# Kernel tuning notes

Hardware: AMD Instinct MI355X
Metric: run time of the kernel (lower is better)

The kernel has to match this reference:

```python
import jax, jax.numpy as jnp
import numpy as np

HIDDEN = 512
QK_DIM = HIDDEN // 8  # 64
B, H, W = 32, 32, 32


def conv1x1(x, w, b):
    # 1x1 conv == channel matmul: w [out_c, in_c], x [b, in_c, h, w]
    return jnp.einsum('oc,bchw->bohw', w, x) + b[None, :, None, None]


def setup_inputs() -> dict:
    key = jax.random.key(0)
    ks = jax.random.split(key, 10)
    s = 0.02
    return {
        'x': jax.random.normal(ks[0], (B, HIDDEN, H, W), jnp.float32),
        'pos_embedding': jax.random.normal(ks[1], (1, HIDDEN, 32, 32), jnp.float32),
        'query_w': jax.random.normal(ks[2], (QK_DIM, HIDDEN), jnp.float32) * s,
        'query_b': jax.random.normal(ks[3], (QK_DIM,), jnp.float32) * s,
        'key_w': jax.random.normal(ks[4], (QK_DIM, HIDDEN), jnp.float32) * s,
        'key_b': jax.random.normal(ks[5], (QK_DIM,), jnp.float32) * s,
        'value_w': jax.random.normal(ks[6], (HIDDEN, HIDDEN), jnp.float32) * s,
        'value_b': jax.random.normal(ks[7], (HIDDEN,), jnp.float32) * s,
        'out_w': jax.random.normal(ks[8], (HIDDEN, HIDDEN), jnp.float32) * s,
        'out_b': jax.random.normal(ks[9], (HIDDEN,), jnp.float32) * s,
    }


def reference(x, pos_embedding, query_w, query_b, key_w, key_b,
              value_w, value_b, out_w, out_b):
    b, c, h, w = x.shape
    n = h * w
    x = x + pos_embedding[:, :, :h, :w]
    q = conv1x1(x, query_w, query_b).reshape(b, -1, n)   # [b, d, n]
    k = conv1x1(x, key_w, key_b).reshape(b, -1, n)       # [b, d, n]
    v = conv1x1(x, value_w, value_b).reshape(b, -1, n)   # [b, c, n]
    # scores[b,i,j] = sum_d q[b,d,i] * k[b,d,j]  (no 1/sqrt(d) scaling, faithful)
    scores = jnp.einsum('bdi,bdj->bij', q, k)
    attn = jax.nn.softmax(scores, axis=-1)               # [b, n, n]
    # out[b,c,i] = sum_j v[b,c,j] * attn[b,i,j]
    out = jnp.einsum('bcj,bij->bci', v, attn).reshape(b, c, h, w)
    return conv1x1(out, out_w, out_b)
```

## Files before the change

kernel.cpp:

```cpp
#include <hip/hip_runtime.h>

#define BB 32
#define CC 512
#define DD 64
#define NN 1024
#define GRP 16
#define NGRP (BB / GRP)

typedef float4 f4;
typedef __attribute__((ext_vector_type(8))) short bf16x8;
typedef __attribute__((ext_vector_type(4))) float f32x4;
typedef __attribute__((ext_vector_type(4))) unsigned short us4;
typedef __attribute__((ext_vector_type(8))) unsigned short us8;

__device__ inline unsigned short bf16rn(float f) {
  union { float f; unsigned u; } v; v.f = f;
  unsigned r = v.u + 0x7fff + ((v.u >> 16) & 1);
  return (unsigned short)(r >> 16);
}

__device__ inline void gl_lds16(const void* g, void* l) {
  __builtin_amdgcn_global_load_lds(
      (const __attribute__((address_space(1))) unsigned int*)g,
      (__attribute__((address_space(3))) unsigned int*)l, 16, 0, 0);
}

__device__ inline void wait_vm0_barrier() {
  asm volatile("s_waitcnt vmcnt(0)" ::: "memory");
  __builtin_amdgcn_s_barrier();
}

__device__ inline int xcd_swz(int bid, int nwg) {
  return (bid & 7) * (nwg >> 3) + (bid >> 3);
}

template <int KDIM>
__device__ inline void gemm_core(const unsigned short* __restrict__ A,
                                 const unsigned short* __restrict__ Bt,
                                 int m0, int n0, int tid,
                                 unsigned short* sA, unsigned short* sB,
                                 f32x4 acc[4][4]) {
  const int wave = tid >> 6, lane = tid & 63;
  const int wm = (wave & 1) * 64, wn = (wave >> 1) * 64;
  const int fm = lane & 15;
  const int kq = lane >> 4;
  const int srow = lane >> 3;
  const int sg   = (lane & 7) ^ srow;

  const unsigned short* ga = A  + (size_t)(m0 + srow) * KDIM + sg * 8;
  const unsigned short* gb = Bt + (size_t)(n0 + srow) * KDIM + sg * 8;

  auto stage = [&](int buf, int k0) {
#pragma unroll
    for (int t = 0; t < 4; ++t) {
      const int R = wave * 32 + t * 8;
      gl_lds16(ga + (size_t)R * KDIM + k0, sA + buf * 8192 + R * 64);
      gl_lds16(gb + (size_t)R * KDIM + k0, sB + buf * 8192 + R * 64);
    }
  };

  stage(0, 0);
  wait_vm0_barrier();

  int cur = 0;
  for (int k0 = 0; k0 < KDIM; k0 += 64) {
    if (k0 + 64 < KDIM) stage(cur ^ 1, k0 + 64);
    const unsigned short* pA = sA + cur * 8192;
    const unsigned short* pB = sB + cur * 8192;
#pragma unroll
    for (int ks = 0; ks < 2; ++ks) {
      bf16x8 af[4], bfr[4];
#pragma unroll
      for (int i = 0; i < 4; ++i) {
        const int ra = wm + i * 16 + fm;
        const int rb = wn + i * 16 + fm;
        af[i]  = *(const bf16x8*)(pA + ra * 64 + ((ks * 4 + kq) ^ (ra & 7)) * 8);
        bfr[i] = *(const bf16x8*)(pB + rb * 64 + ((ks * 4 + kq) ^ (rb & 7)) * 8);
      }
#pragma unroll
      for (int i = 0; i < 4; ++i)
#pragma unroll
        for (int j = 0; j < 4; ++j)
          acc[i][j] = __builtin_amdgcn_mfma_f32_16x16x32_bf16(af[i], bfr[j], acc[i][j], 0, 0, 0);
    }
    wait_vm0_barrier();
    cur ^= 1;
  }
}

__global__ __launch_bounds__(256) void prep_w(
    const float* __restrict__ qw, const float* __restrict__ kw, const float* __restrict__ vw,
    const float* __restrict__ qb, const float* __restrict__ kb, const float* __restrict__ vb,
    const float* __restrict__ ow,
    unsigned short* __restrict__ wcat, unsigned short* __restrict__ owb,
    float* __restrict__ bcat) {
  int idx = blockIdx.x * 256 + threadIdx.x;
  if (idx < 640 * 512) {
    int row = idx >> 9;
    float v = (row < 64) ? qw[idx] : (row < 128) ? kw[idx - 64 * 512] : vw[idx - 128 * 512];
    wcat[idx] = bf16rn(v);
    if (idx < 640) bcat[idx] = (idx < 64) ? qb[idx] : (idx < 128) ? kb[idx - 64] : vb[idx - 128];
  } else {
    int j = idx - 640 * 512;
    owb[j] = bf16rn(ow[j]);
  }
}

__global__ __launch_bounds__(256) void prep_x(const float* __restrict__ x,
                                              const float* __restrict__ pos,
                                              unsigned short* __restrict__ A) {
  __shared__ float t[64][65];
  const int b = blockIdx.z, i0 = blockIdx.x * 64, c0 = blockIdx.y * 64;
  const int tid = threadIdx.x;
  const int ci = tid >> 4, il = (tid & 15) * 4;
  const float* xb = x + (size_t)b * CC * NN;
#pragma unroll
  for (int r = 0; r < 4; ++r) {
    int cl = r * 16 + ci;
    f4 xv = *(const f4*)(xb  + (size_t)(c0 + cl) * NN + i0 + il);
    f4 pv = *(const f4*)(pos + (size_t)(c0 + cl) * NN + i0 + il);
    t[cl][il + 0] = xv.x + pv.x;
    t[cl][il + 1] = xv.y + pv.y;
    t[cl][il + 2] = xv.z + pv.z;
    t[cl][il + 3] = xv.w + pv.w;
  }
  __syncthreads();
  const int iw = tid >> 2, cw = (tid & 3) * 16;
  unsigned short* dst = A + ((size_t)b * NN + i0 + iw) * CC + c0 + cw;
  us8 p0, p1;
#pragma unroll
  for (int j = 0; j < 8; ++j) p0[j] = bf16rn(t[cw + j][iw]);
#pragma unroll
  for (int j = 0; j < 8; ++j) p1[j] = bf16rn(t[cw + 8 + j][iw]);
  *(us8*)dst = p0;
  *(us8*)(dst + 8) = p1;
}

__global__ __launch_bounds__(256) void proj_gemm(
    const unsigned short* __restrict__ A, const unsigned short* __restrict__ wcat,
    const float* __restrict__ bcat,
    unsigned short* __restrict__ qo, unsigned short* __restrict__ ko,
    unsigned short* __restrict__ vto) {
  __shared__ unsigned short sA[16384], sB[16384];
  const int wid = xcd_swz(blockIdx.x, 1280);
  const int m0 = (wid & 7) * 128, n0 = ((wid >> 3) % 5) * 128, b = wid / 40;
  const int tid = threadIdx.x, wave = tid >> 6, lane = tid & 63;
  f32x4 acc[4][4];
#pragma unroll
  for (int i = 0; i < 4; ++i)
#pragma unroll
    for (int j = 0; j < 4; ++j) acc[i][j] = (f32x4)(0.0f);

  gemm_core<512>(A + (size_t)b * NN * CC, wcat, m0, n0, tid, sA, sB, acc);

  const int wm = (wave & 1) * 64, wn = (wave >> 1) * 64;
#pragma unroll
  for (int i = 0; i < 4; ++i)
#pragma unroll
    for (int j = 0; j < 4; ++j) {
      int col  = n0 + wn + j * 16 + (lane & 15);
      int rowb = m0 + wm + i * 16 + (lane >> 4) * 4;
      float bias = bcat[col];
      if (col < 64) {
#pragma unroll
        for (int r = 0; r < 4; ++r)
          qo[((size_t)b * NN + rowb + r) * DD + col] = bf16rn(acc[i][j][r] + bias);
      } else if (col < 128) {
#pragma unroll
        for (int r = 0; r < 4; ++r)
          ko[((size_t)b * NN + rowb + r) * DD + col - 64] = bf16rn(acc[i][j][r] + bias);
      } else {
        int c = col - 128;
        us4 pk;
#pragma unroll
        for (int r = 0; r < 4; ++r) pk[r] = bf16rn(acc[i][j][r] + bias);
        *(us4*)(vto + ((size_t)b * CC + c) * NN + rowb) = pk;
      }
    }
}

__global__ __launch_bounds__(256) void stats_kernel(
    const unsigned short* __restrict__ q, const unsigned short* __restrict__ k,
    float2* __restrict__ stats_part) {
  __shared__ unsigned short sQ[8192];
  __shared__ unsigned short sK[16384];
  __shared__ float2 wred[4][128];

  const int wid = xcd_swz(blockIdx.x, 512);
  const int i0 = (wid & 7) * 128, jc = (wid >> 3) & 1, b = wid >> 4;
  const int jbase = jc * 512;
  const int tid = threadIdx.x, wave = tid >> 6, lane = tid & 63;
  const int wm = (wave & 1) * 64, wn = (wave >> 1) * 64;
  const int fm = lane & 15, kq = lane >> 4;
  const int srow = lane >> 3, sg = (lane & 7) ^ srow;

  const unsigned short* qb = q + (size_t)b * NN * DD;
  const unsigned short* kb = k + (size_t)b * NN * DD;

  auto stageK = [&](int buf, int j0) {
#pragma unroll
    for (int t = 0; t < 4; ++t) {
      const int R = wave * 32 + t * 8;
      gl_lds16(kb + (size_t)(j0 + R + srow) * DD + sg * 8, sK + buf * 8192 + R * 64);
    }
  };

#pragma unroll
  for (int t = 0; t < 4; ++t) {
    const int R = wave * 32 + t * 8;
    gl_lds16(qb + (size_t)(i0 + R + srow) * DD + sg * 8, sQ + R * 64);
  }
  stageK(0, jbase);
  wait_vm0_barrier();

  bf16x8 aq[4][2];
#pragma unroll
  for (int i = 0; i < 4; ++i)
#pragma unroll
    for (int kd = 0; kd < 2; ++kd) {
      const int ra = wm + i * 16 + fm;
      aq[i][kd] = *(const bf16x8*)(sQ + ra * 64 + ((kd * 4 + kq) ^ (ra & 7)) * 8);
    }

  float m_l[4][4], l_l[4][4];
#pragma unroll
  for (int i = 0; i < 4; ++i)
#pragma unroll
    for (int r = 0; r < 4; ++r) { m_l[i][r] = -1e30f; l_l[i][r] = 0.f; }

  int cur = 0;
#pragma unroll
  for (int jt = 0; jt < 4; ++jt) {
    if (jt < 3) stageK(cur ^ 1, jbase + (jt + 1) * 128);
    const unsigned short* pK = sK + cur * 8192;
    f32x4 S[4][4];
#pragma unroll
    for (int i = 0; i < 4; ++i)
#pragma unroll
      for (int j = 0; j < 4; ++j) S[i][j] = (f32x4)(0.0f);
#pragma unroll
    for (int kd = 0; kd < 2; ++kd) {
      bf16x8 bk[4];
#pragma unroll
      for (int j = 0; j < 4; ++j) {
        const int rb = wn + j * 16 + fm;
        bk[j] = *(const bf16x8*)(pK + rb * 64 + ((kd * 4 + kq) ^ (rb & 7)) * 8);
      }
#pragma unroll
      for (int i = 0; i < 4; ++i)
#pragma unroll
        for (int j = 0; j < 4; ++j)
          S[i][j] = __builtin_amdgcn_mfma_f32_16x16x32_bf16(aq[i][kd], bk[j], S[i][j], 0, 0, 0);
    }
#pragma unroll
    for (int i = 0; i < 4; ++i)
#pragma unroll
      for (int r = 0; r < 4; ++r) {
        float v0 = S[i][0][r], v1 = S[i][1][r], v2 = S[i][2][r], v3 = S[i][3][r];
        float mt = fmaxf(fmaxf(v0, v1), fmaxf(v2, v3));
        float lt = __expf(v0 - mt) + __expf(v1 - mt) + __expf(v2 - mt) + __expf(v3 - mt);
        float mo = m_l[i][r];
        float mn = fmaxf(mo, mt);
        l_l[i][r] = l_l[i][r] * __expf(mo - mn) + lt * __expf(mt - mn);
        m_l[i][r] = mn;
      }
    wait_vm0_barrier();
    cur ^= 1;
  }

#pragma unroll
  for (int i = 0; i < 4; ++i)
#pragma unroll
    for (int r = 0; r < 4; ++r) {
      float m = m_l[i][r], l = l_l[i][r];
#pragma unroll
      for (int off = 1; off < 16; off <<= 1) {
        float mo = __shfl_xor(m, off, 64);
        float lo = __shfl_xor(l, off, 64);
        float mn = fmaxf(m, mo);
        l = l * __expf(m - mn) + lo * __expf(mo - mn);
        m = mn;
      }
      m_l[i][r] = m; l_l[i][r] = l;
    }
  if ((lane & 15) == 0) {
#pragma unroll
    for (int i = 0; i < 4; ++i)
#pragma unroll
      for (int r = 0; r < 4; ++r) {
        float2 p; p.x = m_l[i][r]; p.y = l_l[i][r];
        wred[wave][wm + i * 16 + kq * 4 + r] = p;
      }
  }
  __syncthreads();
  if (tid < 128) {
    const int a = tid >> 6;
    float2 p0 = wred[a][tid], p1 = wred[a + 2][tid];
    float mn = fmaxf(p0.x, p1.x);
    float l = p0.y * __expf(p0.x - mn) + p1.y * __expf(p1.x - mn);
    float2 o; o.x = mn; o.y = l;
    stats_part[((size_t)b * NN + i0 + tid) * 2 + jc] = o;
  }
}

__global__ __launch_bounds__(256) void pnorm_kernel(
    const unsigned short* __restrict__ q, const unsigned short* __restrict__ k,
    const float2* __restrict__ stats_part, unsigned short* __restrict__ P) {
  __shared__ unsigned short sQ[8192];
  __shared__ unsigned short sK[8192];

  const int wid = xcd_swz(blockIdx.x, 8 * 8 * GRP);
  const int j0 = (wid & 7) * 128, i0 = ((wid >> 3) & 7) * 128, b = wid >> 6;
  const int tid = threadIdx.x, wave = tid >> 6, lane = tid & 63;
  const int wm = (wave & 1) * 64, wn = (wave >> 1) * 64;
  const int fm = lane & 15, kq = lane >> 4;
  const int srow = lane >> 3, sg = (lane & 7) ^ srow;

  const unsigned short* qb = q + (size_t)b * NN * DD;
  const unsigned short* kb = k + (size_t)b * NN * DD;

#pragma unroll
  for (int t = 0; t < 4; ++t) {
    const int R = wave * 32 + t * 8;
    gl_lds16(qb + (size_t)(i0 + R + srow) * DD + sg * 8, sQ + R * 64);
    gl_lds16(kb + (size_t)(j0 + R + srow) * DD + sg * 8, sK + R * 64);
  }

  float mrow[4][4], irow[4][4];
#pragma unroll
  for (int i = 0; i < 4; ++i)
#pragma unroll
    for (int r = 0; r < 4; ++r) {
      const size_t row = (size_t)b * NN + i0 + wm + i * 16 + kq * 4 + r;
      f4 st = *(const f4*)(stats_part + row * 2);
      float m = fmaxf(st.x, st.z);
      float l = st.y * __expf(st.x - m) + st.w * __expf(st.z - m);
      mrow[i][r] = m; irow[i][r] = 1.0f / l;
    }

  wait_vm0_barrier();

  bf16x8 aq[4][2];
#pragma unroll
  for (int i = 0; i < 4; ++i)
#pragma unroll
    for (int kd = 0; kd < 2; ++kd) {
      const int ra = wm + i * 16 + fm;
      aq[i][kd] = *(const bf16x8*)(sQ + ra * 64 + ((kd * 4 + kq) ^ (ra & 7)) * 8);
    }

  f32x4 S[4][4];
#pragma unroll
  for (int i = 0; i < 4; ++i)
#pragma unroll
    for (int j = 0; j < 4; ++j) S[i][j] = (f32x4)(0.0f);
#pragma unroll
  for (int kd = 0; kd < 2; ++kd) {
    bf16x8 bk[4];
#pragma unroll
    for (int j = 0; j < 4; ++j) {
      const int rb = wn + j * 16 + fm;
      bk[j] = *(const bf16x8*)(sK + rb * 64 + ((kd * 4 + kq) ^ (rb & 7)) * 8);
    }
#pragma unroll
    for (int i = 0; i < 4; ++i)
#pragma unroll
      for (int j = 0; j < 4; ++j)
        S[i][j] = __builtin_amdgcn_mfma_f32_16x16x32_bf16(aq[i][kd], bk[j], S[i][j], 0, 0, 0);
  }
#pragma unroll
  for (int i = 0; i < 4; ++i)
#pragma unroll
    for (int j = 0; j < 4; ++j) {
      const int col = j0 + wn + j * 16 + fm;
#pragma unroll
      for (int r = 0; r < 4; ++r) {
        const int row = i0 + wm + i * 16 + kq * 4 + r;
        P[((size_t)b * NN + row) * NN + col] =
            bf16rn(__expf(S[i][j][r] - mrow[i][r]) * irow[i][r]);
      }
    }
}

__global__ __launch_bounds__(256) void pv_gemm(
    const unsigned short* __restrict__ P, const unsigned short* __restrict__ vT,
    unsigned short* __restrict__ attnout) {
  __shared__ unsigned short sA[16384], sB[16384];
  const int wid = xcd_swz(blockIdx.x, 8 * 4 * GRP);
  const int m0 = (wid & 7) * 128, n0 = ((wid >> 3) & 3) * 128, b = wid >> 5;
  const int tid = threadIdx.x, wave = tid >> 6, lane = tid & 63;
  f32x4 acc[4][4];
#pragma unroll
  for (int i = 0; i < 4; ++i)
#pragma unroll
    for (int j = 0; j < 4; ++j) acc[i][j] = (f32x4)(0.0f);

  gemm_core<1024>(P + (size_t)b * NN * NN, vT + (size_t)b * CC * NN, m0, n0, tid, sA, sB, acc);

  const int wm = (wave & 1) * 64, wn = (wave >> 1) * 64;
#pragma unroll
  for (int i = 0; i < 4; ++i)
#pragma unroll
    for (int j = 0; j < 4; ++j) {
      int col  = n0 + wn + j * 16 + (lane & 15);
      int rowb = m0 + wm + i * 16 + (lane >> 4) * 4;
#pragma unroll
      for (int r = 0; r < 4; ++r)
        attnout[((size_t)b * NN + rowb + r) * CC + col] = bf16rn(acc[i][j][r]);
    }
}

__global__ __launch_bounds__(256) void outproj_gemm(
    const unsigned short* __restrict__ owb, const unsigned short* __restrict__ attnout,
    const float* __restrict__ ob, float* __restrict__ out) {
  __shared__ unsigned short sA[16384], sB[16384];
  const int wid = xcd_swz(blockIdx.x, 1024);
  const int m0 = (wid & 3) * 128, n0 = ((wid >> 2) & 7) * 128, b = wid >> 5;
  const int tid = threadIdx.x, wave = tid >> 6, lane = tid & 63;
  f32x4 acc[4][4];
#pragma unroll
  for (int i = 0; i < 4; ++i)
#pragma unroll
    for (int j = 0; j < 4; ++j) acc[i][j] = (f32x4)(0.0f);

  gemm_core<512>(owb, attnout + (size_t)b * NN * CC, m0, n0, tid, sA, sB, acc);

  const int wm = (wave & 1) * 64, wn = (wave >> 1) * 64;
#pragma unroll
  for (int i = 0; i < 4; ++i)
#pragma unroll
    for (int j = 0; j < 4; ++j) {
      int col  = n0 + wn + j * 16 + (lane & 15);
      int rowb = m0 + wm + i * 16 + (lane >> 4) * 4;
      f4 b4 = *(const f4*)(ob + rowb);
#pragma unroll
      for (int r = 0; r < 4; ++r)
        out[((size_t)b * CC + rowb + r) * NN + col] = acc[i][j][r] + ((const float*)&b4)[r];
    }
}

extern "C" void kernel_launch(void* const* d_in, const int* in_sizes, int n_in,
                              void* d_out, int out_size, void* d_ws, size_t ws_size,
                              hipStream_t stream) {
  const float* x   = (const float*)d_in[0];
  const float* pos = (const float*)d_in[1];
  const float* qw  = (const float*)d_in[2];
  const float* qb  = (const float*)d_in[3];
  const float* kw  = (const float*)d_in[4];
  const float* kb  = (const float*)d_in[5];
  const float* vw  = (const float*)d_in[6];
  const float* vb  = (const float*)d_in[7];
  const float* ow  = (const float*)d_in[8];
  const float* ob  = (const float*)d_in[9];
  float* out = (float*)d_out;

  char* w = (char*)d_ws;
  unsigned short* wcat = (unsigned short*)w; w += (size_t)640 * 512 * 2;
  unsigned short* owb  = (unsigned short*)w; w += (size_t)512 * 512 * 2;
  float*          bcat = (float*)w;          w += 640 * 4;
  unsigned short* A    = (unsigned short*)w; w += (size_t)BB * NN * CC * 2;
  unsigned short* q    = (unsigned short*)w; w += (size_t)BB * NN * DD * 2;
  unsigned short* k    = (unsigned short*)w; w += (size_t)BB * NN * DD * 2;
  unsigned short* vT   = (unsigned short*)w; w += (size_t)BB * CC * NN * 2;
  float2*    stats_prt = (float2*)w;         w += (size_t)BB * NN * 2 * 8;
  unsigned short* PG   = (unsigned short*)w; w += (size_t)GRP * NN * NN * 2;
  unsigned short* attnout = A;

  hipLaunchKernelGGL(prep_w, dim3(2304), dim3(256), 0, stream,
                     qw, kw, vw, qb, kb, vb, ow, wcat, owb, bcat);
  hipLaunchKernelGGL(prep_x, dim3(16, 8, 32), dim3(256), 0, stream, x, pos, A);
  hipLaunchKernelGGL(proj_gemm, dim3(1280), dim3(256), 0, stream,
                     A, wcat, bcat, q, k, vT);
  hipLaunchKernelGGL(stats_kernel, dim3(512), dim3(256), 0, stream, q, k, stats_prt);

  for (int g = 0; g < NGRP; ++g) {
    const unsigned short* qg  = q  + (size_t)g * GRP * NN * DD;
    const unsigned short* kg  = k  + (size_t)g * GRP * NN * DD;
    const unsigned short* vTg = vT + (size_t)g * GRP * CC * NN;
    const float2*         stg = stats_prt + (size_t)g * GRP * NN * 2;
    unsigned short* aog = attnout + (size_t)g * GRP * NN * CC;
    hipLaunchKernelGGL(pnorm_kernel, dim3(8 * 8 * GRP), dim3(256), 0, stream,
                       qg, kg, stg, PG);
    hipLaunchKernelGGL(pv_gemm, dim3(8 * 4 * GRP), dim3(256), 0, stream, PG, vTg, aog);
  }

  hipLaunchKernelGGL(outproj_gemm, dim3(1024), dim3(256), 0, stream,
                     owb, attnout, ob, out);
}
```

Measured before the change: 291.5 us.

## Drop max-subtraction softmax pass; compute exp(QK) once and normalize in PV epilogue

```diff
diff --git a/kernel.cpp b/kernel.cpp
--- a/kernel.cpp
+++ b/kernel.cpp
@@ -179,14 +179,14 @@
     }
 }
 
-__global__ __launch_bounds__(256) void stats_kernel(
+__global__ __launch_bounds__(256) void qkexp_kernel(
     const unsigned short* __restrict__ q, const unsigned short* __restrict__ k,
-    float2* __restrict__ stats_part) {
+    float* __restrict__ lpart, unsigned short* __restrict__ P) {
   __shared__ unsigned short sQ[8192];
   __shared__ unsigned short sK[16384];
-  __shared__ float2 wred[4][128];
-
-  const int wid = xcd_swz(blockIdx.x, 512);
+  __shared__ float wred[4][128];
+
+  const int wid = xcd_swz(blockIdx.x, 8 * 2 * GRP);
   const int i0 = (wid & 7) * 128, jc = (wid >> 3) & 1, b = wid >> 4;
   const int jbase = jc * 512;
   const int tid = threadIdx.x, wave = tid >> 6, lane = tid & 63;
@@ -222,11 +222,7 @@
       aq[i][kd] = *(const bf16x8*)(sQ + ra * 64 + ((kd * 4 + kq) ^ (ra & 7)) * 8);
     }
 
-  float m_l[4][4], l_l[4][4];
-#pragma unroll
-  for (int i = 0; i < 4; ++i)
-#pragma unroll
-    for (int r = 0; r < 4; ++r) { m_l[i][r] = -1e30f; l_l[i][r] = 0.f; }
+  float l_l[4] = {0.f, 0.f, 0.f, 0.f};
 
   int cur = 0;
 #pragma unroll
@@ -235,156 +231,69 @@
     const unsigned short* pK = sK + cur * 8192;
     f32x4 S[4][4];
 #pragma unroll
-    for (int i = 0; i < 4; ++i)
-#pragma unroll
-      for (int j = 0; j < 4; ++j) S[i][j] = (f32x4)(0.0f);
+    for (int jk = 0; jk < 4; ++jk)
+#pragma unroll
+      for (int iq = 0; iq < 4; ++iq) S[jk][iq] = (f32x4)(0.0f);
 #pragma unroll
     for (int kd = 0; kd < 2; ++kd) {
       bf16x8 bk[4];
 #pragma unroll
-      for (int j = 0; j < 4; ++j) {
-        const int rb = wn + j * 16 + fm;
-        bk[j] = *(const bf16x8*)(pK + rb * 64 + ((kd * 4 + kq) ^ (rb & 7)) * 8);
+      for (int jk = 0; jk < 4; ++jk) {
+        const int rb = wn + jk * 16 + fm;
+        bk[jk] = *(const bf16x8*)(pK + rb * 64 + ((kd * 4 + kq) ^ (rb & 7)) * 8);
       }
 #pragma unroll
-      for (int i = 0; i < 4; ++i)
-#pragma unroll
-        for (int j = 0; j < 4; ++j)
-          S[i][j] = __builtin_amdgcn_mfma_f32_16x16x32_bf16(aq[i][kd], bk[j], S[i][j], 0, 0, 0);
-    }
-#pragma unroll
-    for (int i = 0; i < 4; ++i)
-#pragma unroll
-      for (int r = 0; r < 4; ++r) {
-        float v0 = S[i][0][r], v1 = S[i][1][r], v2 = S[i][2][r], v3 = S[i][3][r];
-        float mt = fmaxf(fmaxf(v0, v1), fmaxf(v2, v3));
-        float lt = __expf(v0 - mt) + __expf(v1 - mt) + __expf(v2 - mt) + __expf(v3 - mt);
-        float mo = m_l[i][r];
-        float mn = fmaxf(mo, mt);
-        l_l[i][r] = l_l[i][r] * __expf(mo - mn) + lt * __expf(mt - mn);
-        m_l[i][r] = mn;
+      for (int jk = 0; jk < 4; ++jk)
+#pragma unroll
+        for (int iq = 0; iq < 4; ++iq)
+          S[jk][iq] = __builtin_amdgcn_mfma_f32_16x16x32_bf16(bk[jk], aq[iq][kd], S[jk][iq], 0, 0, 0);
+    }
+    us4 pk[4][4];
+#pragma unroll
+    for (int jk = 0; jk < 4; ++jk)
+#pragma unroll
+      for (int iq = 0; iq < 4; ++iq) {
+#pragma unroll
+        for (int r = 0; r < 4; ++r) {
+          float e = __expf(S[jk][iq][r]);
+          pk[jk][iq][r] = bf16rn(e);
+          l_l[iq] += e;
+        }
       }
     wait_vm0_barrier();
+#pragma unroll
+    for (int jk = 0; jk < 4; ++jk)
+#pragma unroll
+      for (int iq = 0; iq < 4; ++iq) {
+        const int row = i0 + wm + iq * 16 + fm;
+        const int col = jbase + jt * 128 + wn + jk * 16 + kq * 4;
+        *(us4*)(P + ((size_t)b * NN + row) * NN + col) = pk[jk][iq];
+      }
     cur ^= 1;
   }
 
 #pragma unroll
-  for (int i = 0; i < 4; ++i)
-#pragma unroll
-    for (int r = 0; r < 4; ++r) {
-      float m = m_l[i][r], l = l_l[i][r];
-#pragma unroll
-      for (int off = 1; off < 16; off <<= 1) {
-        float mo = __shfl_xor(m, off, 64);
-        float lo = __shfl_xor(l, off, 64);
-        float mn = fmaxf(m, mo);
-        l = l * __expf(m - mn) + lo * __expf(mo - mn);
-        m = mn;
-      }
-      m_l[i][r] = m; l_l[i][r] = l;
-    }
-  if ((lane & 15) == 0) {
-#pragma unroll
-    for (int i = 0; i < 4; ++i)
-#pragma unroll
-      for (int r = 0; r < 4; ++r) {
-        float2 p; p.x = m_l[i][r]; p.y = l_l[i][r];
-        wred[wave][wm + i * 16 + kq * 4 + r] = p;
-      }
+  for (int iq = 0; iq < 4; ++iq) {
+    float l = l_l[iq];
+    l += __shfl_xor(l, 16, 64);
+    l += __shfl_xor(l, 32, 64);
+    l_l[iq] = l;
+  }
+  if (lane < 16) {
+#pragma unroll
+    for (int iq = 0; iq < 4; ++iq) wred[wave][wm + iq * 16 + fm] = l_l[iq];
   }
   __syncthreads();
   if (tid < 128) {
     const int a = tid >> 6;
-    float2 p0 = wred[a][tid], p1 = wred[a + 2][tid];
-    float mn = fmaxf(p0.x, p1.x);
-    float l = p0.y * __expf(p0.x - mn) + p1.y * __expf(p1.x - mn);
-    float2 o; o.x = mn; o.y = l;
-    stats_part[((size_t)b * NN + i0 + tid) * 2 + jc] = o;
-  }
-}
-
-__global__ __launch_bounds__(256) void pnorm_kernel(
-    const unsigned short* __restrict__ q, const unsigned short* __restrict__ k,
-    const float2* __restrict__ stats_part, unsigned short* __restrict__ P) {
-  __shared__ unsigned short sQ[8192];
-  __shared__ unsigned short sK[8192];
-
-  const int wid = xcd_swz(blockIdx.x, 8 * 8 * GRP);
-  const int j0 = (wid & 7) * 128, i0 = ((wid >> 3) & 7) * 128, b = wid >> 6;
-  const int tid = threadIdx.x, wave = tid >> 6, lane = tid & 63;
-  const int wm = (wave & 1) * 64, wn = (wave >> 1) * 64;
-  const int fm = lane & 15, kq = lane >> 4;
-  const int srow = lane >> 3, sg = (lane & 7) ^ srow;
-
-  const unsigned short* qb = q + (size_t)b * NN * DD;
-  const unsigned short* kb = k + (size_t)b * NN * DD;
-
-#pragma unroll
-  for (int t = 0; t < 4; ++t) {
-    const int R = wave * 32 + t * 8;
-    gl_lds16(qb + (size_t)(i0 + R + srow) * DD + sg * 8, sQ + R * 64);
-    gl_lds16(kb + (size_t)(j0 + R + srow) * DD + sg * 8, sK + R * 64);
-  }
-
-  float mrow[4][4], irow[4][4];
-#pragma unroll
-  for (int i = 0; i < 4; ++i)
-#pragma unroll
-    for (int r = 0; r < 4; ++r) {
-      const size_t row = (size_t)b * NN + i0 + wm + i * 16 + kq * 4 + r;
-      f4 st = *(const f4*)(stats_part + row * 2);
-      float m = fmaxf(st.x, st.z);
-      float l = st.y * __expf(st.x - m) + st.w * __expf(st.z - m);
-      mrow[i][r] = m; irow[i][r] = 1.0f / l;
-    }
-
-  wait_vm0_barrier();
-
-  bf16x8 aq[4][2];
-#pragma unroll
-  for (int i = 0; i < 4; ++i)
-#pragma unroll
-    for (int kd = 0; kd < 2; ++kd) {
-      const int ra = wm + i * 16 + fm;
-      aq[i][kd] = *(const bf16x8*)(sQ + ra * 64 + ((kd * 4 + kq) ^ (ra & 7)) * 8);
-    }
-
-  f32x4 S[4][4];
-#pragma unroll
-  for (int i = 0; i < 4; ++i)
-#pragma unroll
-    for (int j = 0; j < 4; ++j) S[i][j] = (f32x4)(0.0f);
-#pragma unroll
-  for (int kd = 0; kd < 2; ++kd) {
-    bf16x8 bk[4];
-#pragma unroll
-    for (int j = 0; j < 4; ++j) {
-      const int rb = wn + j * 16 + fm;
-      bk[j] = *(const bf16x8*)(sK + rb * 64 + ((kd * 4 + kq) ^ (rb & 7)) * 8);
-    }
-#pragma unroll
-    for (int i = 0; i < 4; ++i)
-#pragma unroll
-      for (int j = 0; j < 4; ++j)
-        S[i][j] = __builtin_amdgcn_mfma_f32_16x16x32_bf16(aq[i][kd], bk[j], S[i][j], 0, 0, 0);
-  }
-#pragma unroll
-  for (int i = 0; i < 4; ++i)
-#pragma unroll
-    for (int j = 0; j < 4; ++j) {
-      const int col = j0 + wn + j * 16 + fm;
-#pragma unroll
-      for (int r = 0; r < 4; ++r) {
-        const int row = i0 + wm + i * 16 + kq * 4 + r;
-        P[((size_t)b * NN + row) * NN + col] =
-            bf16rn(__expf(S[i][j][r] - mrow[i][r]) * irow[i][r]);
-      }
-    }
+    float l = wred[a][tid] + wred[a + 2][tid];
+    lpart[((size_t)b * NN + i0 + tid) * 2 + jc] = l;
+  }
 }
 
 __global__ __launch_bounds__(256) void pv_gemm(
     const unsigned short* __restrict__ P, const unsigned short* __restrict__ vT,
-    unsigned short* __restrict__ attnout) {
+    const float* __restrict__ lpart, unsigned short* __restrict__ attnout) {
   __shared__ unsigned short sA[16384], sB[16384];
   const int wid = xcd_swz(blockIdx.x, 8 * 4 * GRP);
   const int m0 = (wid & 7) * 128, n0 = ((wid >> 3) & 3) * 128, b = wid >> 5;
@@ -398,6 +307,15 @@
   gemm_core<1024>(P + (size_t)b * NN * NN, vT + (size_t)b * CC * NN, m0, n0, tid, sA, sB, acc);
 
   const int wm = (wave & 1) * 64, wn = (wave >> 1) * 64;
+  float inv[4][4];
+#pragma unroll
+  for (int i = 0; i < 4; ++i)
+#pragma unroll
+    for (int r = 0; r < 4; ++r) {
+      const int row = m0 + wm + i * 16 + (lane >> 4) * 4 + r;
+      float2 lp = *(const float2*)(lpart + ((size_t)b * NN + row) * 2);
+      inv[i][r] = 1.0f / (lp.x + lp.y);
+    }
 #pragma unroll
   for (int i = 0; i < 4; ++i)
 #pragma unroll
@@ -406,7 +324,7 @@
       int rowb = m0 + wm + i * 16 + (lane >> 4) * 4;
 #pragma unroll
       for (int r = 0; r < 4; ++r)
-        attnout[((size_t)b * NN + rowb + r) * CC + col] = bf16rn(acc[i][j][r]);
+        attnout[((size_t)b * NN + rowb + r) * CC + col] = bf16rn(acc[i][j][r] * inv[i][r]);
     }
 }
 
@@ -462,7 +380,7 @@
   unsigned short* q    = (unsigned short*)w; w += (size_t)BB * NN * DD * 2;
   unsigned short* k    = (unsigned short*)w; w += (size_t)BB * NN * DD * 2;
   unsigned short* vT   = (unsigned short*)w; w += (size_t)BB * CC * NN * 2;
-  float2*    stats_prt = (float2*)w;         w += (size_t)BB * NN * 2 * 8;
+  float*         lpart = (float*)w;          w += (size_t)BB * NN * 2 * 4;
   unsigned short* PG   = (unsigned short*)w; w += (size_t)GRP * NN * NN * 2;
   unsigned short* attnout = A;
 
@@ -471,17 +389,17 @@
   hipLaunchKernelGGL(prep_x, dim3(16, 8, 32), dim3(256), 0, stream, x, pos, A);
   hipLaunchKernelGGL(proj_gemm, dim3(1280), dim3(256), 0, stream,
                      A, wcat, bcat, q, k, vT);
-  hipLaunchKernelGGL(stats_kernel, dim3(512), dim3(256), 0, stream, q, k, stats_prt);
 
   for (int g = 0; g < NGRP; ++g) {
     const unsigned short* qg  = q  + (size_t)g * GRP * NN * DD;
     const unsigned short* kg  = k  + (size_t)g * GRP * NN * DD;
     const unsigned short* vTg = vT + (size_t)g * GRP * CC * NN;
-    const float2*         stg = stats_prt + (size_t)g * GRP * NN * 2;
+    float*                lpg = lpart + (size_t)g * GRP * NN * 2;
     unsigned short* aog = attnout + (size_t)g * GRP * NN * CC;
-    hipLaunchKernelGGL(pnorm_kernel, dim3(8 * 8 * GRP), dim3(256), 0, stream,
-                       qg, kg, stg, PG);
-    hipLaunchKernelGGL(pv_gemm, dim3(8 * 4 * GRP), dim3(256), 0, stream, PG, vTg, aog);
+    hipLaunchKernelGGL(qkexp_kernel, dim3(8 * 2 * GRP), dim3(256), 0, stream,
+                       qg, kg, lpg, PG);
+    hipLaunchKernelGGL(pv_gemm, dim3(8 * 4 * GRP), dim3(256), 0, stream,
+                       PG, vTg, lpg, aog);
   }
 
   hipLaunchKernelGGL(outproj_gemm, dim3(1024), dim3(256), 0, stream,
```

Result: faster. 283.5 us (-2.8%).
